# Performance work log

Hardware: AMD Instinct MI355X
Metric: run time of the kernel (lower is better)

The kernel has to match this reference:

```python
import jax, jax.numpy as jnp
import numpy as np

B, L, H, E, D = 2, 2048, 8, 64, 64

def setup_inputs() -> dict:
    key = jax.random.key(0)
    kq, kk, kv, ks = jax.random.split(key, 4)
    return {
        "queries": jax.random.normal(kq, (B, L, H, E), dtype=jnp.float32),
        "keys": jax.random.normal(kk, (B, L, H, E), dtype=jnp.float32),
        "values": jax.random.normal(kv, (B, L, H, D), dtype=jnp.float32),
        "sigma": jax.random.normal(ks, (B, L, H), dtype=jnp.float32),
    }

def reference(queries, keys, values, sigma):
    b, l, h, e = queries.shape
    scale = 1.0 / np.sqrt(e).astype(np.float32)
    # raw attention scores [B,H,L,S]
    scores = jnp.einsum('blhe,bshe->bhls', queries, keys)
    # strict causal mask (mask j > i)
    causal = jnp.triu(jnp.ones((l, l), dtype=bool), k=1)
    scores = jnp.where(causal[None, None], -jnp.inf, scores)
    attn = scale * scores
    # learned Gaussian prior per query-key distance
    sig = jnp.transpose(sigma, (0, 2, 1))            # [B,H,L]
    sig = jax.nn.sigmoid(sig * 5.0) + 1e-5
    sig = jnp.power(3.0, sig) - 1.0                  # in (0, 2)
    sig = sig[..., None]                             # [B,H,L,1] broadcast over window
    idx = jnp.arange(l, dtype=jnp.float32)
    dist = jnp.abs(idx[:, None] - idx[None, :])      # [L,L]
    inv_sqrt_2pi = 1.0 / np.sqrt(2.0 * np.pi).astype(np.float32)
    prior = (inv_sqrt_2pi / sig) * jnp.exp(-(dist[None, None] ** 2) / (2.0 * sig ** 2))  # [B,H,L,L]
    series = jax.nn.softmax(attn, axis=-1)           # [B,H,L,S]
    V = jnp.einsum('bhls,bshd->blhd', series, values)  # [B,L,H,D]
    sigma_out = jnp.broadcast_to(sig, prior.shape)
    return V, series, prior, sigma_out
```

## Files before the change

### kernel.cpp

```cpp
#include <hip/hip_runtime.h>

#define L_ 2048
#define H_ 8

typedef __attribute__((ext_vector_type(8))) short short8;
typedef __attribute__((ext_vector_type(4))) float f32x4;

static constexpr size_t OFF_S = 2097152;
static constexpr size_t OFF_P = OFF_S + 67108864;
static constexpr size_t OFF_G = OFF_P + 67108864;

static constexpr size_t WS_K = 1u << 20;
static constexpr size_t WS_V = WS_K + (4u << 20);

__device__ __forceinline__ unsigned short f2bf(float x) {
    union { float f; unsigned int u; } c; c.f = x;
    unsigned int u = c.u;
    u += 0x7fffu + ((u >> 16) & 1u);
    return (unsigned short)(u >> 16);
}
__device__ __forceinline__ float bf2f(unsigned short u) {
    union { float f; unsigned int v; } c; c.v = ((unsigned int)u) << 16; return c.f;
}

__device__ __forceinline__ void gld_lds16(const unsigned short* g, unsigned short* l) {
    __builtin_amdgcn_global_load_lds(
        (const __attribute__((address_space(1))) void*)g,
        (__attribute__((address_space(3))) void*)l, 16, 0, 0);
}

__global__ __launch_bounds__(256) void prep(
    const float* __restrict__ k, const float* __restrict__ v,
    unsigned short* __restrict__ wsK, unsigned short* __restrict__ wsV)
{
    const int tid = threadIdx.x;
    const int blk = blockIdx.x;
    __shared__ __attribute__((aligned(16))) unsigned short tr[64][72];
    if (blk < 512) {
        const int bh = blk >> 5, t = blk & 31;
        const int b = bh >> 3, h = bh & 7;
        unsigned short* dst = wsK + (size_t)(bh * 32 + t) * 4096;
        #pragma unroll
        for (int p = 0; p < 2; ++p) {
            const int cid = tid + (p << 8);
            const int r = cid >> 3, c = cid & 7;
            const int j = (t << 6) + r;
            const float4* src = reinterpret_cast<const float4*>(
                k + (((size_t)((b * L_ + j) * H_ + h)) << 6) + (c << 3));
            float4 x0 = src[0], x1 = src[1];
            union { short8 s; unsigned short u[8]; } w;
            w.u[0]=f2bf(x0.x); w.u[1]=f2bf(x0.y); w.u[2]=f2bf(x0.z); w.u[3]=f2bf(x0.w);
            w.u[4]=f2bf(x1.x); w.u[5]=f2bf(x1.y); w.u[6]=f2bf(x1.z); w.u[7]=f2bf(x1.w);
            *reinterpret_cast<short8*>(dst + r * 64 + ((c ^ (r & 7)) << 3)) = w.s;
        }
    } else {
        const int vb = blk - 512;
        const int bh = vb >> 5, t = vb & 31;
        const int b = bh >> 3, h = bh & 7;
        const int col4 = (tid & 15) << 2;
        #pragma unroll
        for (int p = 0; p < 4; ++p) {
            const int r = (tid >> 4) + (p << 4);
            const int j = (t << 6) + r;
            float4 x = *reinterpret_cast<const float4*>(
                v + (((size_t)((b * L_ + j) * H_ + h)) << 6) + col4);
            tr[col4 + 0][r] = f2bf(x.x); tr[col4 + 1][r] = f2bf(x.y);
            tr[col4 + 2][r] = f2bf(x.z); tr[col4 + 3][r] = f2bf(x.w);
        }
        __syncthreads();
        unsigned short* dst = wsV + (size_t)(bh * 32 + t) * 4096;
        #pragma unroll
        for (int p = 0; p < 2; ++p) {
            const int cid = tid + (p << 8);
            const int d = cid >> 3, cj = cid & 7;
            short8 s = *reinterpret_cast<const short8*>(&tr[d][cj << 3]);
            *reinterpret_cast<short8*>(dst + d * 64 + ((cj ^ (d & 7)) << 3)) = s;
        }
    }
}

__global__ __launch_bounds__(256) void attn(
    const float* __restrict__ q,
    const unsigned short* __restrict__ wsK, const unsigned short* __restrict__ wsV,
    float* __restrict__ out, float* __restrict__ ws_inv)
{
    __shared__ __attribute__((aligned(16))) unsigned short Kb[2][4096];
    __shared__ __attribute__((aligned(16))) unsigned short Vb[2][4096];
    __shared__ __attribute__((aligned(16))) unsigned short Pt[16][72];
    __shared__ float l_sums[16];

    const int tid  = threadIdx.x;
    const int wv   = tid >> 6;
    const int lane = tid & 63;
    const int quad = lane >> 4;
    const int l16  = lane & 15;

    const int blk = blockIdx.x;
    const int s   = 127 - (blk >> 4);
    const int bh  = blk & 15;
    const int b   = bh >> 3, h = bh & 7;
    const int i0  = s << 4;

    if (tid < 16) l_sums[tid] = 0.0f;

    short8 a0, a1;
    {
        const float* qr = q + (((size_t)((b * L_ + (i0 + l16)) * H_ + h)) << 6);
        const float4* q4 = reinterpret_cast<const float4*>(qr) + quad * 2;
        float4 x0 = q4[0], x1 = q4[1];
        float4 y0 = q4[8], y1 = q4[9];
        union { short8 v8; unsigned short u[8]; } fa, fb;
        fa.u[0]=f2bf(x0.x); fa.u[1]=f2bf(x0.y); fa.u[2]=f2bf(x0.z); fa.u[3]=f2bf(x0.w);
        fa.u[4]=f2bf(x1.x); fa.u[5]=f2bf(x1.y); fa.u[6]=f2bf(x1.z); fa.u[7]=f2bf(x1.w);
        fb.u[0]=f2bf(y0.x); fb.u[1]=f2bf(y0.y); fb.u[2]=f2bf(y0.z); fb.u[3]=f2bf(y0.w);
        fb.u[4]=f2bf(y1.x); fb.u[5]=f2bf(y1.y); fb.u[6]=f2bf(y1.z); fb.u[7]=f2bf(y1.w);
        a0 = fa.v8; a1 = fb.v8;
    }

    const int ntiles = (s >> 2) + 1;
    const unsigned short* gK = wsK + ((size_t)bh * 32) * 4096;
    const unsigned short* gV = wsV + ((size_t)bh * 32) * 4096;

    #define STAGE(buf, t) do {                                              \
        const unsigned short* _sk = gK + (size_t)(t) * 4096;                \
        const unsigned short* _sv = gV + (size_t)(t) * 4096;                \
        _Pragma("unroll")                                                   \
        for (int _qq = 0; _qq < 2; ++_qq) {                                 \
            const int _off = (wv << 10) + (_qq << 9);                       \
            gld_lds16(_sk + _off + (lane << 3), &Kb[buf][_off]);            \
            gld_lds16(_sv + _off + (lane << 3), &Vb[buf][_off]);            \
        }                                                                   \
    } while (0)

    f32x4 oacc = {0.f, 0.f, 0.f, 0.f};
    float lpart[4] = {0.f, 0.f, 0.f, 0.f};
    float* outS = out + OFF_S;
    const int r = (wv << 4) + l16;

    STAGE(0, 0);
    for (int t = 0; t < ntiles; ++t) {
        const int p = t & 1;
        __syncthreads();
        if (t + 1 < ntiles) STAGE(1 - p, t + 1);
        const int j0 = t << 6;
        short8 b0 = *reinterpret_cast<const short8*>(&Kb[p][r * 64 + ((quad ^ (r & 7)) << 3)]);
        short8 b1 = *reinterpret_cast<const short8*>(&Kb[p][r * 64 + (((quad + 4) ^ (r & 7)) << 3)]);
        f32x4 c4 = {0.f, 0.f, 0.f, 0.f};
        c4 = __builtin_amdgcn_mfma_f32_16x16x32_bf16(a0, b0, c4, 0, 0, 0);
        c4 = __builtin_amdgcn_mfma_f32_16x16x32_bf16(a1, b1, c4, 0, 0, 0);
        const int j = j0 + r;
        #pragma unroll
        for (int rr = 0; rr < 4; ++rr) {
            const int i = i0 + (quad << 2) + rr;
            float pv = (j <= i) ? __expf(c4[rr] * 0.125f - 8.0f) : 0.0f;
            lpart[rr] += pv;
            Pt[(quad << 2) + rr][r] = f2bf(pv);
        }
        __syncthreads();
        short8 pa0 = *reinterpret_cast<const short8*>(&Pt[l16][quad << 3]);
        short8 pa1 = *reinterpret_cast<const short8*>(&Pt[l16][32 + (quad << 3)]);
        short8 vb0 = *reinterpret_cast<const short8*>(&Vb[p][r * 64 + ((quad ^ (r & 7)) << 3)]);
        short8 vb1 = *reinterpret_cast<const short8*>(&Vb[p][r * 64 + (((quad + 4) ^ (r & 7)) << 3)]);
        oacc = __builtin_amdgcn_mfma_f32_16x16x32_bf16(pa0, vb0, oacc, 0, 0, 0);
        oacc = __builtin_amdgcn_mfma_f32_16x16x32_bf16(pa1, vb1, oacc, 0, 0, 0);
        const int srow = tid >> 4, scol = (tid & 15) << 2;
        const unsigned short* pp = &Pt[srow][scol];
        float4 pf = { bf2f(pp[0]), bf2f(pp[1]), bf2f(pp[2]), bf2f(pp[3]) };
        *reinterpret_cast<float4*>(outS + (((size_t)(bh * L_ + i0 + srow)) << 11) + j0 + scol) = pf;
    }
    #undef STAGE

    #pragma unroll
    for (int rr = 0; rr < 4; ++rr) {
        float x = lpart[rr];
        x += __shfl_xor(x, 1); x += __shfl_xor(x, 2);
        x += __shfl_xor(x, 4); x += __shfl_xor(x, 8);
        if (l16 == 0) atomicAdd(&l_sums[(quad << 2) + rr], x);
    }
    __syncthreads();
    #pragma unroll
    for (int rr = 0; rr < 4; ++rr) {
        const int i = i0 + (quad << 2) + rr;
        const float inv = 1.0f / l_sums[(quad << 2) + rr];
        out[(((size_t)((b * L_ + i) * H_ + h)) << 6) + (wv << 4) + l16] = oacc[rr] * inv;
    }
    if (tid < 16) ws_inv[(bh << 11) + i0 + tid] = 1.0f / l_sums[tid];
}

__global__ __launch_bounds__(256) void finish(
    const float* __restrict__ sg, const float* __restrict__ ws_inv,
    float* __restrict__ out)
{
    __shared__ float sA[4], sC2[4], sS[4], sI[4];
    const int tid = threadIdx.x;
    const int g0 = blockIdx.x << 2;
    if (tid < 4) {
        const int g = g0 + tid;
        const int bh = g >> 11, i = g & 2047, b = bh >> 3, h = bh & 7;
        const float x = sg[(size_t)((b * L_ + i) * H_ + h)];
        const float sgm = 1.0f / (1.0f + __expf(-5.0f * x)) + 1e-5f;
        const float sp = expm1f(sgm * 1.0986122886681098f);
        sS[tid] = sp;
        sA[tid] = 0.3989422804014327f / sp;
        sC2[tid] = 0.5f / (sp * sp);
        sI[tid] = ws_inv[g];
    }
    __syncthreads();
    float* outS = out + OFF_S;
    float* outP = out + OFF_P;
    float* outG = out + OFF_G;
    #pragma unroll
    for (int rr = 0; rr < 4; ++rr) {
        const int g = g0 + rr;
        const int i = g & 2047;
        const size_t base = (size_t)g << 11;
        const float A = sA[rr], C2 = sC2[rr], S = sS[rr], I = sI[rr];
        #pragma unroll
        for (int p = 0; p < 2; ++p) {
            const int c = (tid + (p << 8)) << 2;
            const float d0 = (float)(i - c);
            const float d1 = d0 - 1.f, d2 = d0 - 2.f, d3 = d0 - 3.f;
            float4 pr;
            pr.x = A * __expf(-d0 * d0 * C2);
            pr.y = A * __expf(-d1 * d1 * C2);
            pr.z = A * __expf(-d2 * d2 * C2);
            pr.w = A * __expf(-d3 * d3 * C2);
            *reinterpret_cast<float4*>(outP + base + c) = pr;
            float4 sv = {S, S, S, S};
            *reinterpret_cast<float4*>(outG + base + c) = sv;
            float4 se;
            if (c + 3 <= i) {
                se = *reinterpret_cast<const float4*>(outS + base + c);
                se.x *= I; se.y *= I; se.z *= I; se.w *= I;
            } else if (c > i) {
                se.x = 0.f; se.y = 0.f; se.z = 0.f; se.w = 0.f;
            } else {
                const float4 t4 = *reinterpret_cast<const float4*>(outS + base + c);
                se.x = (c     <= i) ? t4.x * I : 0.f;
                se.y = (c + 1 <= i) ? t4.y * I : 0.f;
                se.z = (c + 2 <= i) ? t4.z * I : 0.f;
                se.w = (c + 3 <= i) ? t4.w * I : 0.f;
            }
            *reinterpret_cast<float4*>(outS + base + c) = se;
        }
    }
}

extern "C" void kernel_launch(void* const* d_in, const int* in_sizes, int n_in,
                              void* d_out, int out_size, void* d_ws, size_t ws_size,
                              hipStream_t stream) {
    const float* q  = (const float*)d_in[0];
    const float* k  = (const float*)d_in[1];
    const float* v  = (const float*)d_in[2];
    const float* sg = (const float*)d_in[3];
    float* outp = (float*)d_out;
    float* ws_inv = (float*)d_ws;
    unsigned short* wsK = (unsigned short*)((char*)d_ws + WS_K);
    unsigned short* wsV = (unsigned short*)((char*)d_ws + WS_V);
    prep<<<dim3(1024), dim3(256), 0, stream>>>(k, v, wsK, wsV);
    attn<<<dim3(2048), dim3(256), 0, stream>>>(q, wsK, wsV, outp, ws_inv);
    finish<<<dim3(8192), dim3(256), 0, stream>>>(sg, ws_inv, outp);
}
```

Before: 888.4 us.

## Fuse finish pass into attention kernel, recomputing normalized scores in a second sweep

The separate finish kernel is merged into the attention kernel. Unnormalized scores are no longer written to global memory and then re-read to be scaled. Instead, after the row sums are known, a second pass reloads K from global, recomputes QK^T, and writes normalized probabilities directly. The same pass writes the Gaussian prior and sigma outputs, and zero-fills the masked tail. This removes one 64 MB read and one 64 MB write of the series tensor, plus a kernel launch, at the cost of doubling the QK MFMA work. The series stores are now strided per lane rather than row-coalesced float4 stores.

After: 889.0 us. Within noise of the previous version (+0.1%).

```diff
diff --git a/kernel.cpp b/kernel.cpp
--- a/kernel.cpp
+++ b/kernel.cpp
@@ -18,9 +18,6 @@
     unsigned int u = c.u;
     u += 0x7fffu + ((u >> 16) & 1u);
     return (unsigned short)(u >> 16);
-}
-__device__ __forceinline__ float bf2f(unsigned short u) {
-    union { float f; unsigned int v; } c; c.v = ((unsigned int)u) << 16; return c.f;
 }
 
 __device__ __forceinline__ void gld_lds16(const unsigned short* g, unsigned short* l) {
@@ -79,15 +76,16 @@
     }
 }
 
-__global__ __launch_bounds__(256) void attn(
-    const float* __restrict__ q,
+__global__ __launch_bounds__(256) void fused(
+    const float* __restrict__ q, const float* __restrict__ sg,
     const unsigned short* __restrict__ wsK, const unsigned short* __restrict__ wsV,
-    float* __restrict__ out, float* __restrict__ ws_inv)
+    float* __restrict__ out)
 {
     __shared__ __attribute__((aligned(16))) unsigned short Kb[2][4096];
     __shared__ __attribute__((aligned(16))) unsigned short Vb[2][4096];
     __shared__ __attribute__((aligned(16))) unsigned short Pt[16][72];
     __shared__ float l_sums[16];
+    __shared__ float sA[16], sC2[16], sS[16];
 
     const int tid  = threadIdx.x;
     const int wv   = tid >> 6;
@@ -101,7 +99,16 @@
     const int b   = bh >> 3, h = bh & 7;
     const int i0  = s << 4;
 
-    if (tid < 16) l_sums[tid] = 0.0f;
+    if (tid < 16) {
+        l_sums[tid] = 0.0f;
+        const int i = i0 + tid;
+        const float x = sg[(size_t)((b * L_ + i) * H_ + h)];
+        const float sgm = 1.0f / (1.0f + __expf(-5.0f * x)) + 1e-5f;
+        const float sp  = expm1f(sgm * 1.0986122886681098f);
+        sS[tid]  = sp;
+        sA[tid]  = 0.3989422804014327f / sp;
+        sC2[tid] = 0.5f / (sp * sp);
+    }
 
     short8 a0, a1;
     {
@@ -134,7 +141,6 @@
 
     f32x4 oacc = {0.f, 0.f, 0.f, 0.f};
     float lpart[4] = {0.f, 0.f, 0.f, 0.f};
-    float* outS = out + OFF_S;
     const int r = (wv << 4) + l16;
 
     STAGE(0, 0);
@@ -142,13 +148,12 @@
         const int p = t & 1;
         __syncthreads();
         if (t + 1 < ntiles) STAGE(1 - p, t + 1);
-        const int j0 = t << 6;
         short8 b0 = *reinterpret_cast<const short8*>(&Kb[p][r * 64 + ((quad ^ (r & 7)) << 3)]);
         short8 b1 = *reinterpret_cast<const short8*>(&Kb[p][r * 64 + (((quad + 4) ^ (r & 7)) << 3)]);
         f32x4 c4 = {0.f, 0.f, 0.f, 0.f};
         c4 = __builtin_amdgcn_mfma_f32_16x16x32_bf16(a0, b0, c4, 0, 0, 0);
         c4 = __builtin_amdgcn_mfma_f32_16x16x32_bf16(a1, b1, c4, 0, 0, 0);
-        const int j = j0 + r;
+        const int j = (t << 6) + r;
         #pragma unroll
         for (int rr = 0; rr < 4; ++rr) {
             const int i = i0 + (quad << 2) + rr;
@@ -163,10 +168,6 @@
         short8 vb1 = *reinterpret_cast<const short8*>(&Vb[p][r * 64 + (((quad + 4) ^ (r & 7)) << 3)]);
         oacc = __builtin_amdgcn_mfma_f32_16x16x32_bf16(pa0, vb0, oacc, 0, 0, 0);
         oacc = __builtin_amdgcn_mfma_f32_16x16x32_bf16(pa1, vb1, oacc, 0, 0, 0);
-        const int srow = tid >> 4, scol = (tid & 15) << 2;
-        const unsigned short* pp = &Pt[srow][scol];
-        float4 pf = { bf2f(pp[0]), bf2f(pp[1]), bf2f(pp[2]), bf2f(pp[3]) };
-        *reinterpret_cast<float4*>(outS + (((size_t)(bh * L_ + i0 + srow)) << 11) + j0 + scol) = pf;
     }
     #undef STAGE
 
@@ -178,71 +179,75 @@
         if (l16 == 0) atomicAdd(&l_sums[(quad << 2) + rr], x);
     }
     __syncthreads();
+
+    float inv[4];
+    #pragma unroll
+    for (int rr = 0; rr < 4; ++rr) inv[rr] = 1.0f / l_sums[(quad << 2) + rr];
     #pragma unroll
     for (int rr = 0; rr < 4; ++rr) {
         const int i = i0 + (quad << 2) + rr;
-        const float inv = 1.0f / l_sums[(quad << 2) + rr];
-        out[(((size_t)((b * L_ + i) * H_ + h)) << 6) + (wv << 4) + l16] = oacc[rr] * inv;
-    }
-    if (tid < 16) ws_inv[(bh << 11) + i0 + tid] = 1.0f / l_sums[tid];
-}
-
-__global__ __launch_bounds__(256) void finish(
-    const float* __restrict__ sg, const float* __restrict__ ws_inv,
-    float* __restrict__ out)
-{
-    __shared__ float sA[4], sC2[4], sS[4], sI[4];
-    const int tid = threadIdx.x;
-    const int g0 = blockIdx.x << 2;
-    if (tid < 4) {
-        const int g = g0 + tid;
-        const int bh = g >> 11, i = g & 2047, b = bh >> 3, h = bh & 7;
-        const float x = sg[(size_t)((b * L_ + i) * H_ + h)];
-        const float sgm = 1.0f / (1.0f + __expf(-5.0f * x)) + 1e-5f;
-        const float sp = expm1f(sgm * 1.0986122886681098f);
-        sS[tid] = sp;
-        sA[tid] = 0.3989422804014327f / sp;
-        sC2[tid] = 0.5f / (sp * sp);
-        sI[tid] = ws_inv[g];
-    }
-    __syncthreads();
+        out[(((size_t)((b * L_ + i) * H_ + h)) << 6) + (wv << 4) + l16] = oacc[rr] * inv[rr];
+    }
+
     float* outS = out + OFF_S;
     float* outP = out + OFF_P;
     float* outG = out + OFF_G;
-    #pragma unroll
-    for (int rr = 0; rr < 4; ++rr) {
-        const int g = g0 + rr;
-        const int i = g & 2047;
-        const size_t base = (size_t)g << 11;
-        const float A = sA[rr], C2 = sC2[rr], S = sS[rr], I = sI[rr];
-        #pragma unroll
-        for (int p = 0; p < 2; ++p) {
-            const int c = (tid + (p << 8)) << 2;
-            const float d0 = (float)(i - c);
-            const float d1 = d0 - 1.f, d2 = d0 - 2.f, d3 = d0 - 3.f;
-            float4 pr;
-            pr.x = A * __expf(-d0 * d0 * C2);
-            pr.y = A * __expf(-d1 * d1 * C2);
-            pr.z = A * __expf(-d2 * d2 * C2);
-            pr.w = A * __expf(-d3 * d3 * C2);
-            *reinterpret_cast<float4*>(outP + base + c) = pr;
-            float4 sv = {S, S, S, S};
-            *reinterpret_cast<float4*>(outG + base + c) = sv;
-            float4 se;
-            if (c + 3 <= i) {
-                se = *reinterpret_cast<const float4*>(outS + base + c);
-                se.x *= I; se.y *= I; se.z *= I; se.w *= I;
-            } else if (c > i) {
-                se.x = 0.f; se.y = 0.f; se.z = 0.f; se.w = 0.f;
-            } else {
-                const float4 t4 = *reinterpret_cast<const float4*>(outS + base + c);
-                se.x = (c     <= i) ? t4.x * I : 0.f;
-                se.y = (c + 1 <= i) ? t4.y * I : 0.f;
-                se.z = (c + 2 <= i) ? t4.z * I : 0.f;
-                se.w = (c + 3 <= i) ? t4.w * I : 0.f;
-            }
-            *reinterpret_cast<float4*>(outS + base + c) = se;
-        }
+
+    const int srow = tid >> 4, scol = (tid & 15) << 2;
+    const float Arow = sA[srow], C2r = sC2[srow], Srow = sS[srow];
+    const size_t rowb = ((size_t)(bh * L_ + i0 + srow)) << 11;
+    const float fi = (float)(i0 + srow);
+    const float4 sv = {Srow, Srow, Srow, Srow};
+
+    const int off0 = r * 64 + ((quad ^ (r & 7)) << 3);
+    const int off1 = r * 64 + (((quad + 4) ^ (r & 7)) << 3);
+    float* psb = outS + (((size_t)(bh * L_ + i0 + (quad << 2))) << 11) + r;
+
+    short8 kb0 = *reinterpret_cast<const short8*>(gK + off0);
+    short8 kb1 = *reinterpret_cast<const short8*>(gK + off1);
+    int t = 0;
+    for (; t < ntiles; ++t) {
+        short8 kn0 = kb0, kn1 = kb1;
+        if (t + 1 < ntiles) {
+            const unsigned short* kp = gK + (((size_t)(t + 1)) << 12);
+            kn0 = *reinterpret_cast<const short8*>(kp + off0);
+            kn1 = *reinterpret_cast<const short8*>(kp + off1);
+        }
+        f32x4 c4 = {0.f, 0.f, 0.f, 0.f};
+        c4 = __builtin_amdgcn_mfma_f32_16x16x32_bf16(a0, kb0, c4, 0, 0, 0);
+        c4 = __builtin_amdgcn_mfma_f32_16x16x32_bf16(a1, kb1, c4, 0, 0, 0);
+        const int j = (t << 6) + r;
+        #pragma unroll
+        for (int rr = 0; rr < 4; ++rr) {
+            const int i = i0 + (quad << 2) + rr;
+            const float pv = (j <= i) ? __expf(c4[rr] * 0.125f - 8.0f) * inv[rr] : 0.0f;
+            psb[((size_t)rr << 11) + (t << 6)] = pv;
+        }
+        const int c = (t << 6) + scol;
+        const float d0 = fi - (float)c;
+        const float d1 = d0 - 1.f, d2 = d0 - 2.f, d3 = d0 - 3.f;
+        float4 pr;
+        pr.x = Arow * __expf(-d0 * d0 * C2r);
+        pr.y = Arow * __expf(-d1 * d1 * C2r);
+        pr.z = Arow * __expf(-d2 * d2 * C2r);
+        pr.w = Arow * __expf(-d3 * d3 * C2r);
+        *reinterpret_cast<float4*>(outP + rowb + c) = pr;
+        *reinterpret_cast<float4*>(outG + rowb + c) = sv;
+        kb0 = kn0; kb1 = kn1;
+    }
+    const float4 z4 = {0.f, 0.f, 0.f, 0.f};
+    for (; t < 32; ++t) {
+        const int c = (t << 6) + scol;
+        const float d0 = fi - (float)c;
+        const float d1 = d0 - 1.f, d2 = d0 - 2.f, d3 = d0 - 3.f;
+        float4 pr;
+        pr.x = Arow * __expf(-d0 * d0 * C2r);
+        pr.y = Arow * __expf(-d1 * d1 * C2r);
+        pr.z = Arow * __expf(-d2 * d2 * C2r);
+        pr.w = Arow * __expf(-d3 * d3 * C2r);
+        *reinterpret_cast<float4*>(outS + rowb + c) = z4;
+        *reinterpret_cast<float4*>(outP + rowb + c) = pr;
+        *reinterpret_cast<float4*>(outG + rowb + c) = sv;
     }
 }
 
@@ -254,10 +259,8 @@
     const float* v  = (const float*)d_in[2];
     const float* sg = (const float*)d_in[3];
     float* outp = (float*)d_out;
-    float* ws_inv = (float*)d_ws;
     unsigned short* wsK = (unsigned short*)((char*)d_ws + WS_K);
     unsigned short* wsV = (unsigned short*)((char*)d_ws + WS_V);
     prep<<<dim3(1024), dim3(256), 0, stream>>>(k, v, wsK, wsV);
-    attn<<<dim3(2048), dim3(256), 0, stream>>>(q, wsK, wsV, outp, ws_inv);
-    finish<<<dim3(8192), dim3(256), 0, stream>>>(sg, ws_inv, outp);
-}
+    fused<<<dim3(2048), dim3(256), 0, stream>>>(q, sg, wsK, wsV, outp);
+}
```
